# Kernel optimization log

Hardware: AMD Instinct MI355X
Metric: run time of the kernel (lower is better)

Reference implementation:

```python
import jax, jax.numpy as jnp
import numpy as np

NUM_CLASSES = 1000
FEAT_DIM = 256
N = 262144
ALPHA = 0.5


def setup_inputs() -> dict:
    key = jax.random.key(0)
    k1, k2, k3 = jax.random.split(key, 3)
    x = jax.random.normal(k1, (N, FEAT_DIM), dtype=jnp.float32)
    labels = jax.random.randint(k2, (N,), 0, NUM_CLASSES, dtype=jnp.int64)
    centers = jax.random.normal(k3, (NUM_CLASSES, FEAT_DIM), dtype=jnp.float32)
    return {"x": x, "labels": labels, "centers": centers}


def reference(x, labels, centers):
    # loss: mean euclidean distance to own class center, halved
    centers_batch = centers[labels]                      # [N, D] gather
    dist = jnp.sqrt(jnp.sum((x - centers_batch) ** 2, axis=1))  # [N]
    loss = dist.mean() / 2.0

    # center update (torch.no_grad block): single-pass segment mean
    C = centers.shape[0]
    sums = jax.ops.segment_sum(x, labels, num_segments=C)           # [C, D]
    counts = jax.ops.segment_sum(jnp.ones((x.shape[0],), x.dtype), labels,
                                 num_segments=C)                     # [C]
    # mean(x[mask] - center_i) = mean(x[mask]) - center_i
    mean_x = sums / jnp.maximum(counts, 1.0)[:, None]
    delta = mean_x - centers
    new_centers = jnp.where(counts[:, None] > 0,
                            centers + ALPHA * delta, centers)
    return loss, new_centers
```

## Files before the change

### kernel.cpp

```cpp
#include <hip/hip_runtime.h>
#include <math.h>


#define D 256
#define SETUP_BLOCKS 64
#define SETUP_THREADS 1024
#define MAIN_THREADS 256

__device__ __forceinline__ void grid_barrier(int* bar) {
    __syncthreads();
    if (threadIdx.x == 0) {
        __threadfence();
        atomicAdd(bar, 1);
        while (__hip_atomic_load(bar, __ATOMIC_ACQUIRE, __HIP_MEMORY_SCOPE_AGENT)
               < SETUP_BLOCKS) {
            __builtin_amdgcn_s_sleep(2);
        }
    }
    __syncthreads();
}

__global__ __launch_bounds__(1024) void init_kernel(int* __restrict__ counts,
                                                    int* __restrict__ bars,
                                                    double* __restrict__ lossacc) {
    counts[threadIdx.x] = 0;
    if (threadIdx.x < 3) bars[threadIdx.x] = 0;
    if (threadIdx.x == 0) *lossacc = 0.0;
}

__global__ __launch_bounds__(SETUP_THREADS) void setup_kernel(
        const int* __restrict__ lraw, int n,
        int* __restrict__ counts, int* __restrict__ offsets,
        int* __restrict__ bar0, int* __restrict__ bar1,
        int* __restrict__ hist_all, int* __restrict__ rowidx) {
    __shared__ int sh[1024];
    __shared__ int s_flag;
    const int tid = threadIdx.x;
    const int b = blockIdx.x;

    if (tid == 0) s_flag = 0;
    sh[tid] = 0;
    __syncthreads();
    if (tid < 512 && 2 * tid + 1 < n) {
        if (lraw[2 * tid + 1]) atomicOr(&s_flag, 1);
    }
    __syncthreads();
    const int f64 = (s_flag == 0) ? 1 : 0;

    for (int i = b * SETUP_THREADS + tid; i < n; i += SETUP_BLOCKS * SETUP_THREADS) {
        const int lbl = f64 ? lraw[2 * (size_t)i] : lraw[i];
        atomicAdd(&sh[lbl], 1);
    }
    __syncthreads();
    const int myh = sh[tid];
    hist_all[b * 1024 + tid] = myh;
    if (myh) atomicAdd(&counts[tid], myh);

    grid_barrier(bar0);

    if (b == 0) {
        const int v = counts[tid];
        sh[tid] = v;
        __syncthreads();
        for (int off = 1; off < 1024; off <<= 1) {
            const int add = (tid >= off) ? sh[tid - off] : 0;
            __syncthreads();
            sh[tid] += add;
            __syncthreads();
        }
        offsets[tid] = sh[tid] - v;
    }

    grid_barrier(bar1);

    int base = offsets[tid];
    for (int pb = 0; pb < b; ++pb) base += hist_all[pb * 1024 + tid];
    __syncthreads();
    sh[tid] = base;
    __syncthreads();
    for (int i = b * SETUP_THREADS + tid; i < n; i += SETUP_BLOCKS * SETUP_THREADS) {
        const int lbl = f64 ? lraw[2 * (size_t)i] : lraw[i];
        const int pos = atomicAdd(&sh[lbl], 1);
        rowidx[pos] = i;
    }
}

__global__ __launch_bounds__(MAIN_THREADS) void main_kernel(
        const float* __restrict__ x, const float* __restrict__ centers,
        const int* __restrict__ offsets, const int* __restrict__ counts,
        const int* __restrict__ rowidx, double* __restrict__ lossacc,
        int* __restrict__ done, int n_rows, int n_classes,
        float* __restrict__ out) {
    const int c = blockIdx.x;
    const int tid = threadIdx.x;
    const int wave = tid >> 6;
    const int lane = tid & 63;

    __shared__ float s_sum[4][D];
    __shared__ float s_loss[4];

    const float4 ctr = ((const float4*)(centers + (size_t)c * D))[lane];
    const int start = offsets[c];
    const int cnt = counts[c];

    float4 sum = make_float4(0.f, 0.f, 0.f, 0.f);
    float lsum = 0.f;

    constexpr int U = 4;
    constexpr int WSTR = 4 * U;

    float4 A[U], B[U];
    int nA = 0, nB = 0;

    auto LOAD = [&](int bs, float4* buf) -> int {
        int nv = cnt - bs;
        nv = nv > U ? U : (nv < 0 ? 0 : nv);
        #pragma unroll
        for (int k = 0; k < U; ++k) {
            if (k < nv) {
                const int r = rowidx[start + bs + k];
                buf[k] = ((const float4*)(x + (size_t)r * D))[lane];
            }
        }
        return nv;
    };
    auto PROC = [&](const float4* buf, int nv) {
        #pragma unroll
        for (int k = 0; k < U; ++k) {
            if (k < nv) {
                const float4 v = buf[k];
                sum.x += v.x; sum.y += v.y; sum.z += v.z; sum.w += v.w;
                const float dx = v.x - ctr.x, dy = v.y - ctr.y;
                const float dz = v.z - ctr.z, dw = v.w - ctr.w;
                float sq = dx * dx + dy * dy + dz * dz + dw * dw;
                #pragma unroll
                for (int o = 32; o; o >>= 1) sq += __shfl_xor(sq, o, 64);
                lsum += sqrtf(sq);
            }
        }
    };

    int bs = wave * U;
    nA = LOAD(bs, A); bs += WSTR;
    while (nA) {
        nB = LOAD(bs, B); bs += WSTR;
        PROC(A, nA);
        if (!nB) break;
        nA = LOAD(bs, A); bs += WSTR;
        PROC(B, nB);
    }

    ((float4*)&s_sum[wave][lane * 4])[0] = sum;
    if (lane == 0) s_loss[wave] = lsum;
    __syncthreads();

    const float tot = s_sum[0][tid] + s_sum[1][tid] + s_sum[2][tid] + s_sum[3][tid];
    const float cs = centers[(size_t)c * D + tid];
    float newc = cs;
    if (cnt > 0) {
        const float mean = tot / (float)cnt;
        newc = cs + 0.5f * (mean - cs);
    }
    out[1 + (size_t)c * D + tid] = newc;

    if (tid == 0) {
        const double bl = (double)(s_loss[0] + s_loss[1] + s_loss[2] + s_loss[3]);
        atomicAdd(lossacc, bl);
        __threadfence();
        const int old = atomicAdd(done, 1);
        if (old == n_classes - 1) {
            const double L = atomicAdd(lossacc, 0.0);
            out[0] = (float)(L / (double)n_rows * 0.5);
        }
    }
}

extern "C" void kernel_launch(void* const* d_in, const int* in_sizes, int n_in,
                              void* d_out, int out_size, void* d_ws, size_t ws_size,
                              hipStream_t stream) {
    const float* x       = (const float*)d_in[0];
    const int*   lraw    = (const int*)d_in[1];
    const float* centers = (const float*)d_in[2];
    float* out = (float*)d_out;

    const int n = in_sizes[1];
    const int C = in_sizes[2] / D;

    char* ws = (char*)d_ws;
    int*    counts   = (int*)(ws + 0);
    int*    offsets  = (int*)(ws + 4096);
    int*    bars     = (int*)(ws + 8192);
    double* lossacc  = (double*)(ws + 8208);
    int*    hist_all = (int*)(ws + 16384);
    int*    rowidx   = (int*)(ws + 524288);

    hipLaunchKernelGGL(init_kernel, dim3(1), dim3(1024), 0, stream,
                       counts, bars, lossacc);
    hipLaunchKernelGGL(setup_kernel, dim3(SETUP_BLOCKS), dim3(SETUP_THREADS), 0, stream,
                       lraw, n, counts, offsets, &bars[0], &bars[1], hist_all, rowidx);
    hipLaunchKernelGGL(main_kernel, dim3(C), dim3(MAIN_THREADS), 0, stream,
                       x, centers, offsets, counts, rowidx, lossacc, &bars[2], n, C, out);
}
```

Baseline: 439.4 us.

## Split each class across two blocks with atomic accumulation and a finalize kernel

The main kernel now launches two blocks per class, each handling interleaved 128-row chunks. Row indices are loaded cooperatively once per chunk and broadcast with shuffles, and the unroll depth rises to 8 rows per buffer. Partial sums go into a zeroed float accumulator via atomics, and a new finalize kernel computes the new centers and the loss. This aims to raise parallelism and memory-level parallelism for the gather, at the cost of an extra kernel launch, a zeroing pass, and atomic traffic.

```diff
diff --git a/kernel.cpp b/kernel.cpp
--- a/kernel.cpp
+++ b/kernel.cpp
@@ -6,6 +6,8 @@
 #define SETUP_BLOCKS 64
 #define SETUP_THREADS 1024
 #define MAIN_THREADS 256
+#define CH 128
+#define CPB 2
 
 __device__ __forceinline__ void grid_barrier(int* bar) {
     __syncthreads();
@@ -20,12 +22,18 @@
     __syncthreads();
 }
 
-__global__ __launch_bounds__(1024) void init_kernel(int* __restrict__ counts,
-                                                    int* __restrict__ bars,
-                                                    double* __restrict__ lossacc) {
-    counts[threadIdx.x] = 0;
-    if (threadIdx.x < 3) bars[threadIdx.x] = 0;
-    if (threadIdx.x == 0) *lossacc = 0.0;
+__global__ __launch_bounds__(256) void init_kernel(float* __restrict__ accum,
+                                                   int* __restrict__ counts,
+                                                   int* __restrict__ bars,
+                                                   double* __restrict__ lossacc) {
+    float4* a4 = (float4*)accum;
+    for (int i = blockIdx.x * 256 + threadIdx.x; i < 64000; i += gridDim.x * 256)
+        a4[i] = make_float4(0.f, 0.f, 0.f, 0.f);
+    if (blockIdx.x == 0) {
+        for (int i = threadIdx.x; i < 1024; i += 256) counts[i] = 0;
+        if (threadIdx.x < 3) bars[threadIdx.x] = 0;
+        if (threadIdx.x == 0) *lossacc = 0.0;
+    }
 }
 
 __global__ __launch_bounds__(SETUP_THREADS) void setup_kernel(
@@ -88,10 +96,10 @@
 __global__ __launch_bounds__(MAIN_THREADS) void main_kernel(
         const float* __restrict__ x, const float* __restrict__ centers,
         const int* __restrict__ offsets, const int* __restrict__ counts,
-        const int* __restrict__ rowidx, double* __restrict__ lossacc,
-        int* __restrict__ done, int n_rows, int n_classes,
-        float* __restrict__ out) {
-    const int c = blockIdx.x;
+        const int* __restrict__ rowidx,
+        float* __restrict__ accum, double* __restrict__ lossacc) {
+    const int c = blockIdx.x / CPB;
+    const int p = blockIdx.x % CPB;
     const int tid = threadIdx.x;
     const int wave = tid >> 6;
     const int lane = tid & 63;
@@ -106,48 +114,55 @@
     float4 sum = make_float4(0.f, 0.f, 0.f, 0.f);
     float lsum = 0.f;
 
-    constexpr int U = 4;
-    constexpr int WSTR = 4 * U;
-
-    float4 A[U], B[U];
-    int nA = 0, nB = 0;
-
-    auto LOAD = [&](int bs, float4* buf) -> int {
-        int nv = cnt - bs;
-        nv = nv > U ? U : (nv < 0 ? 0 : nv);
-        #pragma unroll
-        for (int k = 0; k < U; ++k) {
-            if (k < nv) {
-                const int r = rowidx[start + bs + k];
-                buf[k] = ((const float4*)(x + (size_t)r * D))[lane];
+    for (int cb = p * CH; cb < cnt; cb += CPB * CH) {
+        const int len = min(CH, cnt - cb);
+        const int lo = start + cb;
+        const int i0 = (lane < len) ? rowidx[lo + lane] : 0;
+        const int i1 = (64 + lane < len) ? rowidx[lo + 64 + lane] : 0;
+        const int nw = (len > wave) ? ((len - wave + 3) >> 2) : 0;
+
+        constexpr int U = 8;
+        float4 A[U], B[U];
+
+        auto LOADB = [&](int bb, float4* buf) -> int {
+            int nv = nw - bb * U;
+            nv = nv < 0 ? 0 : (nv > U ? U : nv);
+            #pragma unroll
+            for (int k = 0; k < U; ++k) {
+                if (k < nv) {
+                    const int pos = wave + 4 * (bb * U + k);
+                    const int r = __shfl(pos < 64 ? i0 : i1, pos & 63, 64);
+                    buf[k] = ((const float4*)(x + (size_t)r * D))[lane];
+                }
             }
+            return nv;
+        };
+        auto PROC = [&](const float4* buf, int nv) {
+            #pragma unroll
+            for (int k = 0; k < U; ++k) {
+                if (k < nv) {
+                    const float4 v = buf[k];
+                    sum.x += v.x; sum.y += v.y; sum.z += v.z; sum.w += v.w;
+                    const float dx = v.x - ctr.x, dy = v.y - ctr.y;
+                    const float dz = v.z - ctr.z, dw = v.w - ctr.w;
+                    float sq = dx * dx + dy * dy + dz * dz + dw * dw;
+                    #pragma unroll
+                    for (int o = 32; o; o >>= 1) sq += __shfl_xor(sq, o, 64);
+                    lsum += sqrtf(sq);
+                }
+            }
+        };
+
+        int bb = 0;
+        int nA = LOADB(0, A);
+        while (nA) {
+            const int nB = LOADB(bb + 1, B);
+            PROC(A, nA);
+            if (!nB) break;
+            nA = LOADB(bb + 2, A);
+            PROC(B, nB);
+            bb += 2;
         }
-        return nv;
-    };
-    auto PROC = [&](const float4* buf, int nv) {
-        #pragma unroll
-        for (int k = 0; k < U; ++k) {
-            if (k < nv) {
-                const float4 v = buf[k];
-                sum.x += v.x; sum.y += v.y; sum.z += v.z; sum.w += v.w;
-                const float dx = v.x - ctr.x, dy = v.y - ctr.y;
-                const float dz = v.z - ctr.z, dw = v.w - ctr.w;
-                float sq = dx * dx + dy * dy + dz * dz + dw * dw;
-                #pragma unroll
-                for (int o = 32; o; o >>= 1) sq += __shfl_xor(sq, o, 64);
-                lsum += sqrtf(sq);
-            }
-        }
-    };
-
-    int bs = wave * U;
-    nA = LOAD(bs, A); bs += WSTR;
-    while (nA) {
-        nB = LOAD(bs, B); bs += WSTR;
-        PROC(A, nA);
-        if (!nB) break;
-        nA = LOAD(bs, A); bs += WSTR;
-        PROC(B, nB);
     }
 
     ((float4*)&s_sum[wave][lane * 4])[0] = sum;
@@ -155,24 +170,25 @@
     __syncthreads();
 
     const float tot = s_sum[0][tid] + s_sum[1][tid] + s_sum[2][tid] + s_sum[3][tid];
-    const float cs = centers[(size_t)c * D + tid];
-    float newc = cs;
-    if (cnt > 0) {
-        const float mean = tot / (float)cnt;
-        newc = cs + 0.5f * (mean - cs);
-    }
-    out[1 + (size_t)c * D + tid] = newc;
-
+    atomicAdd(&accum[(size_t)c * D + tid], tot);
     if (tid == 0) {
         const double bl = (double)(s_loss[0] + s_loss[1] + s_loss[2] + s_loss[3]);
         atomicAdd(lossacc, bl);
-        __threadfence();
-        const int old = atomicAdd(done, 1);
-        if (old == n_classes - 1) {
-            const double L = atomicAdd(lossacc, 0.0);
-            out[0] = (float)(L / (double)n_rows * 0.5);
-        }
-    }
+    }
+}
+
+__global__ __launch_bounds__(256) void finalize_kernel(
+        const float* __restrict__ accum, const float* __restrict__ centers,
+        const int* __restrict__ counts, const double* __restrict__ lossacc,
+        int n, float* __restrict__ out) {
+    const int c = blockIdx.x;
+    const int t = threadIdx.x;
+    const int cnt = counts[c];
+    const float cs = centers[(size_t)c * D + t];
+    const float s = accum[(size_t)c * D + t];
+    const float o = (cnt > 0) ? cs + 0.5f * (s / (float)cnt - cs) : cs;
+    out[1 + (size_t)c * D + t] = o;
+    if (c == 0 && t == 0) out[0] = (float)(*lossacc / (double)n * 0.5);
 }
 
 extern "C" void kernel_launch(void* const* d_in, const int* in_sizes, int n_in,
@@ -193,11 +209,14 @@
     double* lossacc  = (double*)(ws + 8208);
     int*    hist_all = (int*)(ws + 16384);
     int*    rowidx   = (int*)(ws + 524288);
-
-    hipLaunchKernelGGL(init_kernel, dim3(1), dim3(1024), 0, stream,
-                       counts, bars, lossacc);
+    float*  accum    = (float*)(ws + 2097152);
+
+    hipLaunchKernelGGL(init_kernel, dim3(128), dim3(256), 0, stream,
+                       accum, counts, bars, lossacc);
     hipLaunchKernelGGL(setup_kernel, dim3(SETUP_BLOCKS), dim3(SETUP_THREADS), 0, stream,
                        lraw, n, counts, offsets, &bars[0], &bars[1], hist_all, rowidx);
-    hipLaunchKernelGGL(main_kernel, dim3(C), dim3(MAIN_THREADS), 0, stream,
-                       x, centers, offsets, counts, rowidx, lossacc, &bars[2], n, C, out);
-}
+    hipLaunchKernelGGL(main_kernel, dim3(C * CPB), dim3(MAIN_THREADS), 0, stream,
+                       x, centers, offsets, counts, rowidx, accum, lossacc);
+    hipLaunchKernelGGL(finalize_kernel, dim3(C), dim3(256), 0, stream,
+                       accum, centers, counts, lossacc, n, out);
+}
```

After: 421.2 us. -4.1%, faster.
